# Kernel optimization log

Measured on AMD Instinct MI355X. Metric: run time of the kernel, lower is better.

## Reference

```python
import jax, jax.numpy as jnp
import numpy as np

EMBED = 1024
HEAD = 64
CTX = 2048


def setup_inputs() -> dict:
    key = jax.random.key(0)
    ks = jax.random.split(key, 7)
    scale = 1.0 / np.sqrt(EMBED)
    return {
        "x": jax.random.normal(ks[0], (8, CTX, EMBED), dtype=jnp.float32),
        "Wq": jax.random.normal(ks[1], (EMBED, HEAD), dtype=jnp.float32) * scale,
        "bq": jax.random.normal(ks[2], (HEAD,), dtype=jnp.float32) * 0.01,
        "Wk": jax.random.normal(ks[3], (EMBED, HEAD), dtype=jnp.float32) * scale,
        "bk": jax.random.normal(ks[4], (HEAD,), dtype=jnp.float32) * 0.01,
        "Wv": jax.random.normal(ks[5], (EMBED, HEAD), dtype=jnp.float32) * scale,
        "bv": jax.random.normal(ks[6], (HEAD,), dtype=jnp.float32) * 0.01,
    }


def reference(x, Wq, bq, Wk, bk, Wv, bv):
    # x: [B, T, E]
    q = x @ Wq + bq  # [B, T, H]
    k = x @ Wk + bk
    v = x @ Wv + bv
    scores = jnp.einsum("bqh,bkh->bqk", q, k) / jnp.sqrt(jnp.float32(HEAD))
    T = x.shape[1]
    causal = jnp.tril(jnp.ones((T, T), dtype=bool))
    scores = jnp.where(causal, scores, -jnp.inf)
    attn = jax.nn.softmax(scores, axis=-1)  # dropout=0.0 -> identity
    out = jnp.einsum("bqk,bkh->bqh", attn, v)
    return out
```

## Files before the change

### kernel.cpp

```cpp
#include <hip/hip_runtime.h>
#include <math.h>
#include <stdint.h>

#define BDIM 8
#define TDIM 2048
#define EDIM 1024
#define HDIM 64
#define NCHUNK 144

typedef short bf16x8 __attribute__((ext_vector_type(8)));
typedef float f32x4 __attribute__((ext_vector_type(4)));

__device__ __forceinline__ unsigned short f2bf(float f) {
    uint32_t u = __builtin_bit_cast(uint32_t, f);
    u += 0x7fffu + ((u >> 16) & 1u);
    return (unsigned short)(u >> 16);
}

__global__ __launch_bounds__(256) void prep_w(
    const float* __restrict__ Wq, const float* __restrict__ Wk,
    const float* __restrict__ Wv,
    unsigned short* __restrict__ WqT, unsigned short* __restrict__ WkT,
    unsigned short* __restrict__ WvT)
{
    int id = blockIdx.x * 256 + threadIdx.x;
    int e = id >> 6, h = id & 63;
    int oi = h * EDIM + e;
    WqT[oi] = f2bf(Wq[id]);
    WkT[oi] = f2bf(Wk[id]);
    WvT[oi] = f2bf(Wv[id]);
}

__global__ __launch_bounds__(256) void proj_kernel(
    const float* __restrict__ x,
    const unsigned short* __restrict__ WqT, const unsigned short* __restrict__ WkT,
    const unsigned short* __restrict__ WvT,
    const float* __restrict__ bq, const float* __restrict__ bk,
    const float* __restrict__ bv,
    unsigned short* __restrict__ Qb, unsigned short* __restrict__ Kb,
    unsigned short* __restrict__ VbT)
{
    __shared__ unsigned short Xs[2][64][72];
    __shared__ unsigned short Wqs[2][64][72];
    __shared__ unsigned short Wks[2][64][72];
    __shared__ unsigned short Wvs[2][64][72];

    const int t = threadIdx.x;
    const int lane = t & 63, w = t >> 6, quad = lane >> 4, ln = lane & 15;
    const int row0 = blockIdx.x * 64;
    const int sr = t >> 2;
    const int sc = (t & 3) << 4;

    f32x4 accq[4], acck[4], accv[4];
#pragma unroll
    for (int j = 0; j < 4; ++j) {
        accq[j] = (f32x4)(0.f); acck[j] = (f32x4)(0.f); accv[j] = (f32x4)(0.f);
    }

    const float*          xp0 = &x[(size_t)(row0 + sr) * EDIM + sc];
    const unsigned short* wp  = (const unsigned short*)0;
    const size_t wrow = (size_t)sr * EDIM + sc;

    {
        float4 x0 = *(const float4*)(xp0);
        float4 x1 = *(const float4*)(xp0 + 4);
        float4 x2 = *(const float4*)(xp0 + 8);
        float4 x3 = *(const float4*)(xp0 + 12);
        bf16x8 xb0, xb1;
        xb0[0]=(short)f2bf(x0.x); xb0[1]=(short)f2bf(x0.y); xb0[2]=(short)f2bf(x0.z); xb0[3]=(short)f2bf(x0.w);
        xb0[4]=(short)f2bf(x1.x); xb0[5]=(short)f2bf(x1.y); xb0[6]=(short)f2bf(x1.z); xb0[7]=(short)f2bf(x1.w);
        xb1[0]=(short)f2bf(x2.x); xb1[1]=(short)f2bf(x2.y); xb1[2]=(short)f2bf(x2.z); xb1[3]=(short)f2bf(x2.w);
        xb1[4]=(short)f2bf(x3.x); xb1[5]=(short)f2bf(x3.y); xb1[6]=(short)f2bf(x3.z); xb1[7]=(short)f2bf(x3.w);
        *(bf16x8*)&Xs[0][sr][sc]     = xb0;
        *(bf16x8*)&Xs[0][sr][sc + 8] = xb1;
        *(bf16x8*)&Wqs[0][sr][sc]     = *(const bf16x8*)&WqT[wrow];
        *(bf16x8*)&Wqs[0][sr][sc + 8] = *(const bf16x8*)&WqT[wrow + 8];
        *(bf16x8*)&Wks[0][sr][sc]     = *(const bf16x8*)&WkT[wrow];
        *(bf16x8*)&Wks[0][sr][sc + 8] = *(const bf16x8*)&WkT[wrow + 8];
        *(bf16x8*)&Wvs[0][sr][sc]     = *(const bf16x8*)&WvT[wrow];
        *(bf16x8*)&Wvs[0][sr][sc + 8] = *(const bf16x8*)&WvT[wrow + 8];
    }

    for (int kt = 0; kt < EDIM / 64; ++kt) {
        const int cur = kt & 1, nxt = cur ^ 1;

        float4 x0, x1, x2, x3;
        bf16x8 wq0, wq1, wk0, wk1, wv0, wv1;
        if (kt < 15) {
            const float* xp = xp0 + (kt + 1) * 64;
            x0 = *(const float4*)(xp);
            x1 = *(const float4*)(xp + 4);
            x2 = *(const float4*)(xp + 8);
            x3 = *(const float4*)(xp + 12);
            const size_t wo = wrow + (kt + 1) * 64;
            wq0 = *(const bf16x8*)&WqT[wo];
            wq1 = *(const bf16x8*)&WqT[wo + 8];
            wk0 = *(const bf16x8*)&WkT[wo];
            wk1 = *(const bf16x8*)&WkT[wo + 8];
            wv0 = *(const bf16x8*)&WvT[wo];
            wv1 = *(const bf16x8*)&WvT[wo + 8];
        }

        __syncthreads();

        bf16x8 xa0 = *(const bf16x8*)&Xs[cur][16 * w + ln][8 * quad];
        bf16x8 xa1 = *(const bf16x8*)&Xs[cur][16 * w + ln][32 + 8 * quad];
#pragma unroll
        for (int j = 0; j < 4; ++j) {
            bf16x8 w0, w1;
            w0 = *(const bf16x8*)&Wqs[cur][16 * j + ln][8 * quad];
            w1 = *(const bf16x8*)&Wqs[cur][16 * j + ln][32 + 8 * quad];
            accq[j] = __builtin_amdgcn_mfma_f32_16x16x32_bf16(xa0, w0, accq[j], 0, 0, 0);
            accq[j] = __builtin_amdgcn_mfma_f32_16x16x32_bf16(xa1, w1, accq[j], 0, 0, 0);
            w0 = *(const bf16x8*)&Wks[cur][16 * j + ln][8 * quad];
            w1 = *(const bf16x8*)&Wks[cur][16 * j + ln][32 + 8 * quad];
            acck[j] = __builtin_amdgcn_mfma_f32_16x16x32_bf16(xa0, w0, acck[j], 0, 0, 0);
            acck[j] = __builtin_amdgcn_mfma_f32_16x16x32_bf16(xa1, w1, acck[j], 0, 0, 0);
            w0 = *(const bf16x8*)&Wvs[cur][16 * j + ln][8 * quad];
            w1 = *(const bf16x8*)&Wvs[cur][16 * j + ln][32 + 8 * quad];
            accv[j] = __builtin_amdgcn_mfma_f32_16x16x32_bf16(xa0, w0, accv[j], 0, 0, 0);
            accv[j] = __builtin_amdgcn_mfma_f32_16x16x32_bf16(xa1, w1, accv[j], 0, 0, 0);
        }

        if (kt < 15) {
            bf16x8 xb0, xb1;
            xb0[0]=(short)f2bf(x0.x); xb0[1]=(short)f2bf(x0.y); xb0[2]=(short)f2bf(x0.z); xb0[3]=(short)f2bf(x0.w);
            xb0[4]=(short)f2bf(x1.x); xb0[5]=(short)f2bf(x1.y); xb0[6]=(short)f2bf(x1.z); xb0[7]=(short)f2bf(x1.w);
            xb1[0]=(short)f2bf(x2.x); xb1[1]=(short)f2bf(x2.y); xb1[2]=(short)f2bf(x2.z); xb1[3]=(short)f2bf(x2.w);
            xb1[4]=(short)f2bf(x3.x); xb1[5]=(short)f2bf(x3.y); xb1[6]=(short)f2bf(x3.z); xb1[7]=(short)f2bf(x3.w);
            *(bf16x8*)&Xs[nxt][sr][sc]     = xb0;
            *(bf16x8*)&Xs[nxt][sr][sc + 8] = xb1;
            *(bf16x8*)&Wqs[nxt][sr][sc]     = wq0;
            *(bf16x8*)&Wqs[nxt][sr][sc + 8] = wq1;
            *(bf16x8*)&Wks[nxt][sr][sc]     = wk0;
            *(bf16x8*)&Wks[nxt][sr][sc + 8] = wk1;
            *(bf16x8*)&Wvs[nxt][sr][sc]     = wv0;
            *(bf16x8*)&Wvs[nxt][sr][sc + 8] = wv1;
        }
    }

#pragma unroll
    for (int j = 0; j < 4; ++j) {
        int col = 16 * j + ln;
        float bqv = bq[col], bkv = bk[col], bvv = bv[col];
#pragma unroll
        for (int r = 0; r < 4; ++r) {
            size_t row = (size_t)(row0 + 16 * w + 4 * quad + r);
            Qb[row * HDIM + col] = f2bf(accq[j][r] + bqv);
            Kb[row * HDIM + col] = f2bf(acck[j][r] + bkv);
            int bb = (int)(row >> 11);
            int tr = (int)(row & 2047);
            VbT[((size_t)bb * HDIM + col) * TDIM + tr] = f2bf(accv[j][r] + bvv);
        }
    }
}

__global__ __launch_bounds__(256) void attn_partial(
    const unsigned short* __restrict__ Qb, const unsigned short* __restrict__ Kb,
    const unsigned short* __restrict__ VbT,
    float* __restrict__ PO, float* __restrict__ Pm, float* __restrict__ Pl)
{
    __shared__ unsigned short Ks[64][72];
    __shared__ unsigned short VsT[64][72];
    __shared__ unsigned short Ps[64][72];

    const int t = threadIdx.x;
    const int lane = t & 63, w = t >> 6, quad = lane >> 4, ln = lane & 15;
    const int f = blockIdx.x;
    const int b = blockIdx.y;

    int g = 0;
    while (f >= 2 * (g + 1) * (g + 2)) ++g;
    const int r_  = f - 2 * g * (g + 1);
    const int iq  = 4 * g + r_ / (g + 1);
    const int ch  = r_ % (g + 1);

    const int q0 = iq * 64;
    const size_t base = (size_t)b * TDIM * HDIM;
    const int sr = t >> 2;
    const int sc = (t & 3) << 4;

    const size_t qrow = base + (size_t)(q0 + 16 * w + ln) * HDIM;
    bf16x8 qa0 = *(const bf16x8*)&Qb[qrow + 8 * quad];
    bf16x8 qa1 = *(const bf16x8*)&Qb[qrow + 32 + 8 * quad];

    f32x4 od[4];
#pragma unroll
    for (int j = 0; j < 4; ++j) od[j] = (f32x4)(0.f);
    float mrow[4], lrow[4];
#pragma unroll
    for (int r = 0; r < 4; ++r) { mrow[r] = -INFINITY; lrow[r] = 0.f; }

    const float scale = 0.125f;
    int j1 = 4 * ch + 3; if (j1 > iq) j1 = iq;

    for (int jt = 4 * ch; jt <= j1; ++jt) {
        __syncthreads();
        {
            size_t ko = base + (size_t)(jt * 64 + sr) * HDIM + sc;
            *(bf16x8*)&Ks[sr][sc]     = *(const bf16x8*)&Kb[ko];
            *(bf16x8*)&Ks[sr][sc + 8] = *(const bf16x8*)&Kb[ko + 8];
            const unsigned short* vrow =
                &VbT[((size_t)b * HDIM + sr) * TDIM + jt * 64 + sc];
            *(bf16x8*)&VsT[sr][sc]     = *(const bf16x8*)vrow;
            *(bf16x8*)&VsT[sr][sc + 8] = *(const bf16x8*)(vrow + 8);
        }
        __syncthreads();

        f32x4 s[4];
#pragma unroll
        for (int j = 0; j < 4; ++j) {
            bf16x8 kb0 = *(const bf16x8*)&Ks[16 * j + ln][8 * quad];
            bf16x8 kb1 = *(const bf16x8*)&Ks[16 * j + ln][32 + 8 * quad];
            s[j] = (f32x4)(0.f);
            s[j] = __builtin_amdgcn_mfma_f32_16x16x32_bf16(qa0, kb0, s[j], 0, 0, 0);
            s[j] = __builtin_amdgcn_mfma_f32_16x16x32_bf16(qa1, kb1, s[j], 0, 0, 0);
        }

        if (jt == iq) {
#pragma unroll
            for (int j = 0; j < 4; ++j) {
                int kg = jt * 64 + 16 * j + ln;
#pragma unroll
                for (int r = 0; r < 4; ++r) {
                    int qg = q0 + 16 * w + 4 * quad + r;
                    s[j][r] = (kg <= qg) ? s[j][r] * scale : -INFINITY;
                }
            }
        } else {
#pragma unroll
            for (int j = 0; j < 4; ++j)
#pragma unroll
                for (int r = 0; r < 4; ++r) s[j][r] *= scale;
        }

        float mx[4];
#pragma unroll
        for (int r = 0; r < 4; ++r)
            mx[r] = fmaxf(fmaxf(s[0][r], s[1][r]), fmaxf(s[2][r], s[3][r]));
#pragma unroll
        for (int d = 1; d < 16; d <<= 1)
#pragma unroll
            for (int r = 0; r < 4; ++r)
                mx[r] = fmaxf(mx[r], __shfl_xor(mx[r], d));

        float al[4], rs[4];
#pragma unroll
        for (int r = 0; r < 4; ++r) {
            float mn = fmaxf(mrow[r], mx[r]);
            al[r] = __expf(mrow[r] - mn);
            mrow[r] = mn;
            float p0 = __expf(s[0][r] - mn);
            float p1 = __expf(s[1][r] - mn);
            float p2 = __expf(s[2][r] - mn);
            float p3 = __expf(s[3][r] - mn);
            s[0][r] = p0; s[1][r] = p1; s[2][r] = p2; s[3][r] = p3;
            rs[r] = (p0 + p1) + (p2 + p3);
        }
#pragma unroll
        for (int d = 1; d < 16; d <<= 1)
#pragma unroll
            for (int r = 0; r < 4; ++r)
                rs[r] += __shfl_xor(rs[r], d);
#pragma unroll
        for (int r = 0; r < 4; ++r) lrow[r] = lrow[r] * al[r] + rs[r];

#pragma unroll
        for (int j = 0; j < 4; ++j)
#pragma unroll
            for (int r = 0; r < 4; ++r) {
                od[j][r] *= al[r];
                Ps[16 * w + 4 * quad + r][16 * j + ln] = f2bf(s[j][r]);
            }

        bf16x8 pa0 = *(const bf16x8*)&Ps[16 * w + ln][8 * quad];
        bf16x8 pa1 = *(const bf16x8*)&Ps[16 * w + ln][32 + 8 * quad];
#pragma unroll
        for (int j = 0; j < 4; ++j) {
            bf16x8 vb0 = *(const bf16x8*)&VsT[16 * j + ln][8 * quad];
            bf16x8 vb1 = *(const bf16x8*)&VsT[16 * j + ln][32 + 8 * quad];
            od[j] = __builtin_amdgcn_mfma_f32_16x16x32_bf16(pa0, vb0, od[j], 0, 0, 0);
            od[j] = __builtin_amdgcn_mfma_f32_16x16x32_bf16(pa1, vb1, od[j], 0, 0, 0);
        }
    }

    const size_t p = (size_t)b * NCHUNK + f;
#pragma unroll
    for (int j = 0; j < 4; ++j)
#pragma unroll
        for (int r = 0; r < 4; ++r)
            PO[p * 4096 + (size_t)(16 * w + 4 * quad + r) * 64 + 16 * j + ln] = od[j][r];
    if (ln == 0) {
#pragma unroll
        for (int r = 0; r < 4; ++r) {
            Pm[p * 64 + 16 * w + 4 * quad + r] = mrow[r];
            Pl[p * 64 + 16 * w + 4 * quad + r] = lrow[r];
        }
    }
}

__global__ __launch_bounds__(256) void attn_combine(
    const float* __restrict__ PO, const float* __restrict__ Pm,
    const float* __restrict__ Pl, float* __restrict__ out)
{
    const int iq = blockIdx.x, b = blockIdx.y;
    const int g = iq >> 2;
    const int nch = g + 1;
    const int fbase = 2 * g * (g + 1) + (iq - 4 * g) * (g + 1);
    const int t = threadIdx.x;
    const int row = t >> 2;
    const int c0 = (t & 3) << 4;
    const size_t pbase = (size_t)b * NCHUNK + fbase;

    float M = -INFINITY;
    for (int c = 0; c < nch; ++c)
        M = fmaxf(M, Pm[(pbase + c) * 64 + row]);

    float4 a0 = {0,0,0,0}, a1 = {0,0,0,0}, a2 = {0,0,0,0}, a3 = {0,0,0,0};
    float L = 0.f;
    for (int c = 0; c < nch; ++c) {
        size_t p = pbase + c;
        float sc = __expf(Pm[p * 64 + row] - M);
        L += sc * Pl[p * 64 + row];
        const float* po = &PO[p * 4096 + (size_t)row * 64 + c0];
        float4 v0 = *(const float4*)(po);
        float4 v1 = *(const float4*)(po + 4);
        float4 v2 = *(const float4*)(po + 8);
        float4 v3 = *(const float4*)(po + 12);
        a0.x += sc*v0.x; a0.y += sc*v0.y; a0.z += sc*v0.z; a0.w += sc*v0.w;
        a1.x += sc*v1.x; a1.y += sc*v1.y; a1.z += sc*v1.z; a1.w += sc*v1.w;
        a2.x += sc*v2.x; a2.y += sc*v2.y; a2.z += sc*v2.z; a2.w += sc*v2.w;
        a3.x += sc*v3.x; a3.y += sc*v3.y; a3.z += sc*v3.z; a3.w += sc*v3.w;
    }
    float li = 1.f / L;
    a0.x*=li; a0.y*=li; a0.z*=li; a0.w*=li;
    a1.x*=li; a1.y*=li; a1.z*=li; a1.w*=li;
    a2.x*=li; a2.y*=li; a2.z*=li; a2.w*=li;
    a3.x*=li; a3.y*=li; a3.z*=li; a3.w*=li;
    float* op = &out[((size_t)b * TDIM + (size_t)iq * 64 + row) * HDIM + c0];
    *(float4*)(op)      = a0;
    *(float4*)(op + 4)  = a1;
    *(float4*)(op + 8)  = a2;
    *(float4*)(op + 12) = a3;
}

extern "C" void kernel_launch(void* const* d_in, const int* in_sizes, int n_in,
                              void* d_out, int out_size, void* d_ws, size_t ws_size,
                              hipStream_t stream) {
    const float* x  = (const float*)d_in[0];
    const float* Wq = (const float*)d_in[1];
    const float* bq = (const float*)d_in[2];
    const float* Wk = (const float*)d_in[3];
    const float* bk = (const float*)d_in[4];
    const float* Wv = (const float*)d_in[5];
    const float* bv = (const float*)d_in[6];
    float* out = (float*)d_out;

    const size_t n = (size_t)BDIM * TDIM * HDIM;
    unsigned short* Qb  = (unsigned short*)d_ws;
    unsigned short* Kb  = Qb + n;
    unsigned short* VbT = Kb + n;
    unsigned short* WqT = VbT + n;
    unsigned short* WkT = WqT + (size_t)EDIM * HDIM;
    unsigned short* WvT = WkT + (size_t)EDIM * HDIM;
    float* PO = (float*)(WvT + (size_t)EDIM * HDIM);
    float* Pm = PO + (size_t)BDIM * NCHUNK * 4096;
    float* Pl = Pm + (size_t)BDIM * NCHUNK * 64;

    prep_w<<<dim3(EDIM * HDIM / 256), 256, 0, stream>>>(Wq, Wk, Wv, WqT, WkT, WvT);
    proj_kernel<<<dim3(BDIM * TDIM / 64), 256, 0, stream>>>(
        x, WqT, WkT, WvT, bq, bk, bv, Qb, Kb, VbT);
    attn_partial<<<dim3(NCHUNK, BDIM), 256, 0, stream>>>(Qb, Kb, VbT, PO, Pm, Pl);
    attn_combine<<<dim3(TDIM / 64, BDIM), 256, 0, stream>>>(PO, Pm, Pl, out);
}
```

Before: 151.3 us.

## Split projection across Q/K/V blocks and store partial outputs in bf16

The projection kernel now launches three times as many blocks, each computing only one of Q, K or V for a 64-row tile. This cuts shared memory and registers per block and raises parallelism, but x is read and converted three times. Separately, the partial attention outputs are written as bf16 instead of fp32, halving the partial-output write and read traffic in the combine kernel at some cost in precision.

```diff
diff --git a/kernel.cpp b/kernel.cpp
--- a/kernel.cpp
+++ b/kernel.cpp
@@ -15,6 +15,10 @@
     uint32_t u = __builtin_bit_cast(uint32_t, f);
     u += 0x7fffu + ((u >> 16) & 1u);
     return (unsigned short)(u >> 16);
+}
+__device__ __forceinline__ float bf2f(unsigned short s) {
+    uint32_t u = ((uint32_t)s) << 16;
+    return __builtin_bit_cast(float, u);
 }
 
 __global__ __launch_bounds__(256) void prep_w(
@@ -41,24 +45,23 @@
     unsigned short* __restrict__ VbT)
 {
     __shared__ unsigned short Xs[2][64][72];
-    __shared__ unsigned short Wqs[2][64][72];
-    __shared__ unsigned short Wks[2][64][72];
-    __shared__ unsigned short Wvs[2][64][72];
+    __shared__ unsigned short Ws[2][64][72];
 
     const int t = threadIdx.x;
     const int lane = t & 63, w = t >> 6, quad = lane >> 4, ln = lane & 15;
-    const int row0 = blockIdx.x * 64;
+    const int which = blockIdx.x % 3;
+    const int row0  = (blockIdx.x / 3) * 64;
     const int sr = t >> 2;
     const int sc = (t & 3) << 4;
 
-    f32x4 accq[4], acck[4], accv[4];
-#pragma unroll
-    for (int j = 0; j < 4; ++j) {
-        accq[j] = (f32x4)(0.f); acck[j] = (f32x4)(0.f); accv[j] = (f32x4)(0.f);
-    }
-
-    const float*          xp0 = &x[(size_t)(row0 + sr) * EDIM + sc];
-    const unsigned short* wp  = (const unsigned short*)0;
+    const unsigned short* WT = (which == 0) ? WqT : (which == 1) ? WkT : WvT;
+    const float* bias        = (which == 0) ? bq  : (which == 1) ? bk  : bv;
+
+    f32x4 acc[4];
+#pragma unroll
+    for (int j = 0; j < 4; ++j) acc[j] = (f32x4)(0.f);
+
+    const float* xp0  = &x[(size_t)(row0 + sr) * EDIM + sc];
     const size_t wrow = (size_t)sr * EDIM + sc;
 
     {
@@ -73,19 +76,15 @@
         xb1[4]=(short)f2bf(x3.x); xb1[5]=(short)f2bf(x3.y); xb1[6]=(short)f2bf(x3.z); xb1[7]=(short)f2bf(x3.w);
         *(bf16x8*)&Xs[0][sr][sc]     = xb0;
         *(bf16x8*)&Xs[0][sr][sc + 8] = xb1;
-        *(bf16x8*)&Wqs[0][sr][sc]     = *(const bf16x8*)&WqT[wrow];
-        *(bf16x8*)&Wqs[0][sr][sc + 8] = *(const bf16x8*)&WqT[wrow + 8];
-        *(bf16x8*)&Wks[0][sr][sc]     = *(const bf16x8*)&WkT[wrow];
-        *(bf16x8*)&Wks[0][sr][sc + 8] = *(const bf16x8*)&WkT[wrow + 8];
-        *(bf16x8*)&Wvs[0][sr][sc]     = *(const bf16x8*)&WvT[wrow];
-        *(bf16x8*)&Wvs[0][sr][sc + 8] = *(const bf16x8*)&WvT[wrow + 8];
+        *(bf16x8*)&Ws[0][sr][sc]     = *(const bf16x8*)&WT[wrow];
+        *(bf16x8*)&Ws[0][sr][sc + 8] = *(const bf16x8*)&WT[wrow + 8];
     }
 
     for (int kt = 0; kt < EDIM / 64; ++kt) {
         const int cur = kt & 1, nxt = cur ^ 1;
 
         float4 x0, x1, x2, x3;
-        bf16x8 wq0, wq1, wk0, wk1, wv0, wv1;
+        bf16x8 wv0, wv1;
         if (kt < 15) {
             const float* xp = xp0 + (kt + 1) * 64;
             x0 = *(const float4*)(xp);
@@ -93,12 +92,8 @@
             x2 = *(const float4*)(xp + 8);
             x3 = *(const float4*)(xp + 12);
             const size_t wo = wrow + (kt + 1) * 64;
-            wq0 = *(const bf16x8*)&WqT[wo];
-            wq1 = *(const bf16x8*)&WqT[wo + 8];
-            wk0 = *(const bf16x8*)&WkT[wo];
-            wk1 = *(const bf16x8*)&WkT[wo + 8];
-            wv0 = *(const bf16x8*)&WvT[wo];
-            wv1 = *(const bf16x8*)&WvT[wo + 8];
+            wv0 = *(const bf16x8*)&WT[wo];
+            wv1 = *(const bf16x8*)&WT[wo + 8];
         }
 
         __syncthreads();
@@ -107,19 +102,10 @@
         bf16x8 xa1 = *(const bf16x8*)&Xs[cur][16 * w + ln][32 + 8 * quad];
 #pragma unroll
         for (int j = 0; j < 4; ++j) {
-            bf16x8 w0, w1;
-            w0 = *(const bf16x8*)&Wqs[cur][16 * j + ln][8 * quad];
-            w1 = *(const bf16x8*)&Wqs[cur][16 * j + ln][32 + 8 * quad];
-            accq[j] = __builtin_amdgcn_mfma_f32_16x16x32_bf16(xa0, w0, accq[j], 0, 0, 0);
-            accq[j] = __builtin_amdgcn_mfma_f32_16x16x32_bf16(xa1, w1, accq[j], 0, 0, 0);
-            w0 = *(const bf16x8*)&Wks[cur][16 * j + ln][8 * quad];
-            w1 = *(const bf16x8*)&Wks[cur][16 * j + ln][32 + 8 * quad];
-            acck[j] = __builtin_amdgcn_mfma_f32_16x16x32_bf16(xa0, w0, acck[j], 0, 0, 0);
-            acck[j] = __builtin_amdgcn_mfma_f32_16x16x32_bf16(xa1, w1, acck[j], 0, 0, 0);
-            w0 = *(const bf16x8*)&Wvs[cur][16 * j + ln][8 * quad];
-            w1 = *(const bf16x8*)&Wvs[cur][16 * j + ln][32 + 8 * quad];
-            accv[j] = __builtin_amdgcn_mfma_f32_16x16x32_bf16(xa0, w0, accv[j], 0, 0, 0);
-            accv[j] = __builtin_amdgcn_mfma_f32_16x16x32_bf16(xa1, w1, accv[j], 0, 0, 0);
+            bf16x8 w0 = *(const bf16x8*)&Ws[cur][16 * j + ln][8 * quad];
+            bf16x8 w1 = *(const bf16x8*)&Ws[cur][16 * j + ln][32 + 8 * quad];
+            acc[j] = __builtin_amdgcn_mfma_f32_16x16x32_bf16(xa0, w0, acc[j], 0, 0, 0);
+            acc[j] = __builtin_amdgcn_mfma_f32_16x16x32_bf16(xa1, w1, acc[j], 0, 0, 0);
         }
 
         if (kt < 15) {
@@ -130,27 +116,28 @@
             xb1[4]=(short)f2bf(x3.x); xb1[5]=(short)f2bf(x3.y); xb1[6]=(short)f2bf(x3.z); xb1[7]=(short)f2bf(x3.w);
             *(bf16x8*)&Xs[nxt][sr][sc]     = xb0;
             *(bf16x8*)&Xs[nxt][sr][sc + 8] = xb1;
-            *(bf16x8*)&Wqs[nxt][sr][sc]     = wq0;
-            *(bf16x8*)&Wqs[nxt][sr][sc + 8] = wq1;
-            *(bf16x8*)&Wks[nxt][sr][sc]     = wk0;
-            *(bf16x8*)&Wks[nxt][sr][sc + 8] = wk1;
-            *(bf16x8*)&Wvs[nxt][sr][sc]     = wv0;
-            *(bf16x8*)&Wvs[nxt][sr][sc + 8] = wv1;
+            *(bf16x8*)&Ws[nxt][sr][sc]     = wv0;
+            *(bf16x8*)&Ws[nxt][sr][sc + 8] = wv1;
         }
     }
 
 #pragma unroll
     for (int j = 0; j < 4; ++j) {
         int col = 16 * j + ln;
-        float bqv = bq[col], bkv = bk[col], bvv = bv[col];
+        float bv_ = bias[col];
 #pragma unroll
         for (int r = 0; r < 4; ++r) {
             size_t row = (size_t)(row0 + 16 * w + 4 * quad + r);
-            Qb[row * HDIM + col] = f2bf(accq[j][r] + bqv);
-            Kb[row * HDIM + col] = f2bf(acck[j][r] + bkv);
-            int bb = (int)(row >> 11);
-            int tr = (int)(row & 2047);
-            VbT[((size_t)bb * HDIM + col) * TDIM + tr] = f2bf(accv[j][r] + bvv);
+            unsigned short val = f2bf(acc[j][r] + bv_);
+            if (which == 0) {
+                Qb[row * HDIM + col] = val;
+            } else if (which == 1) {
+                Kb[row * HDIM + col] = val;
+            } else {
+                int bb = (int)(row >> 11);
+                int tr = (int)(row & 2047);
+                VbT[((size_t)bb * HDIM + col) * TDIM + tr] = val;
+            }
         }
     }
 }
@@ -158,7 +145,7 @@
 __global__ __launch_bounds__(256) void attn_partial(
     const unsigned short* __restrict__ Qb, const unsigned short* __restrict__ Kb,
     const unsigned short* __restrict__ VbT,
-    float* __restrict__ PO, float* __restrict__ Pm, float* __restrict__ Pl)
+    unsigned short* __restrict__ PO, float* __restrict__ Pm, float* __restrict__ Pl)
 {
     __shared__ unsigned short Ks[64][72];
     __shared__ unsigned short VsT[64][72];
@@ -289,7 +276,8 @@
     for (int j = 0; j < 4; ++j)
 #pragma unroll
         for (int r = 0; r < 4; ++r)
-            PO[p * 4096 + (size_t)(16 * w + 4 * quad + r) * 64 + 16 * j + ln] = od[j][r];
+            PO[p * 4096 + (size_t)(16 * w + 4 * quad + r) * 64 + 16 * j + ln] =
+                f2bf(od[j][r]);
     if (ln == 0) {
 #pragma unroll
         for (int r = 0; r < 4; ++r) {
@@ -300,7 +288,7 @@
 }
 
 __global__ __launch_bounds__(256) void attn_combine(
-    const float* __restrict__ PO, const float* __restrict__ Pm,
+    const unsigned short* __restrict__ PO, const float* __restrict__ Pm,
     const float* __restrict__ Pl, float* __restrict__ out)
 {
     const int iq = blockIdx.x, b = blockIdx.y;
@@ -316,32 +304,34 @@
     for (int c = 0; c < nch; ++c)
         M = fmaxf(M, Pm[(pbase + c) * 64 + row]);
 
-    float4 a0 = {0,0,0,0}, a1 = {0,0,0,0}, a2 = {0,0,0,0}, a3 = {0,0,0,0};
+    float a[16];
+#pragma unroll
+    for (int i = 0; i < 16; ++i) a[i] = 0.f;
     float L = 0.f;
     for (int c = 0; c < nch; ++c) {
         size_t p = pbase + c;
         float sc = __expf(Pm[p * 64 + row] - M);
         L += sc * Pl[p * 64 + row];
-        const float* po = &PO[p * 4096 + (size_t)row * 64 + c0];
-        float4 v0 = *(const float4*)(po);
-        float4 v1 = *(const float4*)(po + 4);
-        float4 v2 = *(const float4*)(po + 8);
-        float4 v3 = *(const float4*)(po + 12);
-        a0.x += sc*v0.x; a0.y += sc*v0.y; a0.z += sc*v0.z; a0.w += sc*v0.w;
-        a1.x += sc*v1.x; a1.y += sc*v1.y; a1.z += sc*v1.z; a1.w += sc*v1.w;
-        a2.x += sc*v2.x; a2.y += sc*v2.y; a2.z += sc*v2.z; a2.w += sc*v2.w;
-        a3.x += sc*v3.x; a3.y += sc*v3.y; a3.z += sc*v3.z; a3.w += sc*v3.w;
+        const unsigned short* po = &PO[p * 4096 + (size_t)row * 64 + c0];
+        bf16x8 v0 = *(const bf16x8*)(po);
+        bf16x8 v1 = *(const bf16x8*)(po + 8);
+#pragma unroll
+        for (int i = 0; i < 8; ++i) {
+            a[i]     += sc * bf2f((unsigned short)v0[i]);
+            a[8 + i] += sc * bf2f((unsigned short)v1[i]);
+        }
     }
     float li = 1.f / L;
-    a0.x*=li; a0.y*=li; a0.z*=li; a0.w*=li;
-    a1.x*=li; a1.y*=li; a1.z*=li; a1.w*=li;
-    a2.x*=li; a2.y*=li; a2.z*=li; a2.w*=li;
-    a3.x*=li; a3.y*=li; a3.z*=li; a3.w*=li;
+    float4 o0, o1, o2, o3;
+    o0.x=a[0]*li;  o0.y=a[1]*li;  o0.z=a[2]*li;  o0.w=a[3]*li;
+    o1.x=a[4]*li;  o1.y=a[5]*li;  o1.z=a[6]*li;  o1.w=a[7]*li;
+    o2.x=a[8]*li;  o2.y=a[9]*li;  o2.z=a[10]*li; o2.w=a[11]*li;
+    o3.x=a[12]*li; o3.y=a[13]*li; o3.z=a[14]*li; o3.w=a[15]*li;
     float* op = &out[((size_t)b * TDIM + (size_t)iq * 64 + row) * HDIM + c0];
-    *(float4*)(op)      = a0;
-    *(float4*)(op + 4)  = a1;
-    *(float4*)(op + 8)  = a2;
-    *(float4*)(op + 12) = a3;
+    *(float4*)(op)      = o0;
+    *(float4*)(op + 4)  = o1;
+    *(float4*)(op + 8)  = o2;
+    *(float4*)(op + 12) = o3;
 }
 
 extern "C" void kernel_launch(void* const* d_in, const int* in_sizes, int n_in,
@@ -363,12 +353,12 @@
     unsigned short* WqT = VbT + n;
     unsigned short* WkT = WqT + (size_t)EDIM * HDIM;
     unsigned short* WvT = WkT + (size_t)EDIM * HDIM;
-    float* PO = (float*)(WvT + (size_t)EDIM * HDIM);
-    float* Pm = PO + (size_t)BDIM * NCHUNK * 4096;
+    unsigned short* PO  = WvT + (size_t)EDIM * HDIM;
+    float* Pm = (float*)(PO + (size_t)BDIM * NCHUNK * 4096);
     float* Pl = Pm + (size_t)BDIM * NCHUNK * 64;
 
     prep_w<<<dim3(EDIM * HDIM / 256), 256, 0, stream>>>(Wq, Wk, Wv, WqT, WkT, WvT);
-    proj_kernel<<<dim3(BDIM * TDIM / 64), 256, 0, stream>>>(
+    proj_kernel<<<dim3(3 * BDIM * TDIM / 64), 256, 0, stream>>>(
         x, WqT, WkT, WvT, bq, bk, bv, Qb, Kb, VbT);
     attn_partial<<<dim3(NCHUNK, BDIM), 256, 0, stream>>>(Qb, Kb, VbT, PO, Pm, Pl);
     attn_combine<<<dim3(TDIM / 64, BDIM), 256, 0, stream>>>(PO, Pm, Pl, out);
```

After: 155.8 us. 1.03x slower.

## Double-buffer K/V tiles in attention and store partial outputs as bf16

Applied to the files above, without the earlier changes.

Attention partial kernel now prefetches the next K/V tile into registers and writes it to a second LDS buffer after the compute, removing one barrier per tile and overlapping global loads with MFMA work. Partial output accumulators are stored as bf16 instead of fp32, halving the write and read traffic between the partial and combine kernels. This costs some precision in the partial outputs and doubles K/V shared memory.

```diff
diff --git a/kernel.cpp b/kernel.cpp
--- a/kernel.cpp
+++ b/kernel.cpp
@@ -15,6 +15,10 @@
     uint32_t u = __builtin_bit_cast(uint32_t, f);
     u += 0x7fffu + ((u >> 16) & 1u);
     return (unsigned short)(u >> 16);
+}
+__device__ __forceinline__ float bf2f(unsigned short s) {
+    uint32_t u = ((uint32_t)s) << 16;
+    return __builtin_bit_cast(float, u);
 }
 
 __global__ __launch_bounds__(256) void prep_w(
@@ -57,8 +61,7 @@
         accq[j] = (f32x4)(0.f); acck[j] = (f32x4)(0.f); accv[j] = (f32x4)(0.f);
     }
 
-    const float*          xp0 = &x[(size_t)(row0 + sr) * EDIM + sc];
-    const unsigned short* wp  = (const unsigned short*)0;
+    const float* xp0  = &x[(size_t)(row0 + sr) * EDIM + sc];
     const size_t wrow = (size_t)sr * EDIM + sc;
 
     {
@@ -158,10 +161,10 @@
 __global__ __launch_bounds__(256) void attn_partial(
     const unsigned short* __restrict__ Qb, const unsigned short* __restrict__ Kb,
     const unsigned short* __restrict__ VbT,
-    float* __restrict__ PO, float* __restrict__ Pm, float* __restrict__ Pl)
+    unsigned short* __restrict__ PO, float* __restrict__ Pm, float* __restrict__ Pl)
 {
-    __shared__ unsigned short Ks[64][72];
-    __shared__ unsigned short VsT[64][72];
+    __shared__ unsigned short Ks[2][64][72];
+    __shared__ unsigned short VsT[2][64][72];
     __shared__ unsigned short Ps[64][72];
 
     const int t = threadIdx.x;
@@ -192,26 +195,40 @@
     for (int r = 0; r < 4; ++r) { mrow[r] = -INFINITY; lrow[r] = 0.f; }
 
     const float scale = 0.125f;
-    int j1 = 4 * ch + 3; if (j1 > iq) j1 = iq;
-
-    for (int jt = 4 * ch; jt <= j1; ++jt) {
+    const int jt0 = 4 * ch;
+    int j1 = jt0 + 3; if (j1 > iq) j1 = iq;
+
+    {
+        size_t ko = base + (size_t)(jt0 * 64 + sr) * HDIM + sc;
+        *(bf16x8*)&Ks[0][sr][sc]     = *(const bf16x8*)&Kb[ko];
+        *(bf16x8*)&Ks[0][sr][sc + 8] = *(const bf16x8*)&Kb[ko + 8];
+        const unsigned short* vrow =
+            &VbT[((size_t)b * HDIM + sr) * TDIM + jt0 * 64 + sc];
+        *(bf16x8*)&VsT[0][sr][sc]     = *(const bf16x8*)vrow;
+        *(bf16x8*)&VsT[0][sr][sc + 8] = *(const bf16x8*)(vrow + 8);
+    }
+
+    for (int jt = jt0; jt <= j1; ++jt) {
+        const int cur = (jt - jt0) & 1, nxt = cur ^ 1;
+
+        bf16x8 kn0, kn1, vn0, vn1;
+        if (jt < j1) {
+            size_t ko = base + (size_t)((jt + 1) * 64 + sr) * HDIM + sc;
+            kn0 = *(const bf16x8*)&Kb[ko];
+            kn1 = *(const bf16x8*)&Kb[ko + 8];
+            const unsigned short* vrow =
+                &VbT[((size_t)b * HDIM + sr) * TDIM + (jt + 1) * 64 + sc];
+            vn0 = *(const bf16x8*)vrow;
+            vn1 = *(const bf16x8*)(vrow + 8);
+        }
+
         __syncthreads();
-        {
-            size_t ko = base + (size_t)(jt * 64 + sr) * HDIM + sc;
-            *(bf16x8*)&Ks[sr][sc]     = *(const bf16x8*)&Kb[ko];
-            *(bf16x8*)&Ks[sr][sc + 8] = *(const bf16x8*)&Kb[ko + 8];
-            const unsigned short* vrow =
-                &VbT[((size_t)b * HDIM + sr) * TDIM + jt * 64 + sc];
-            *(bf16x8*)&VsT[sr][sc]     = *(const bf16x8*)vrow;
-            *(bf16x8*)&VsT[sr][sc + 8] = *(const bf16x8*)(vrow + 8);
-        }
-        __syncthreads();
 
         f32x4 s[4];
 #pragma unroll
         for (int j = 0; j < 4; ++j) {
-            bf16x8 kb0 = *(const bf16x8*)&Ks[16 * j + ln][8 * quad];
-            bf16x8 kb1 = *(const bf16x8*)&Ks[16 * j + ln][32 + 8 * quad];
+            bf16x8 kb0 = *(const bf16x8*)&Ks[cur][16 * j + ln][8 * quad];
+            bf16x8 kb1 = *(const bf16x8*)&Ks[cur][16 * j + ln][32 + 8 * quad];
             s[j] = (f32x4)(0.f);
             s[j] = __builtin_amdgcn_mfma_f32_16x16x32_bf16(qa0, kb0, s[j], 0, 0, 0);
             s[j] = __builtin_amdgcn_mfma_f32_16x16x32_bf16(qa1, kb1, s[j], 0, 0, 0);
@@ -277,11 +294,18 @@
         bf16x8 pa1 = *(const bf16x8*)&Ps[16 * w + ln][32 + 8 * quad];
 #pragma unroll
         for (int j = 0; j < 4; ++j) {
-            bf16x8 vb0 = *(const bf16x8*)&VsT[16 * j + ln][8 * quad];
-            bf16x8 vb1 = *(const bf16x8*)&VsT[16 * j + ln][32 + 8 * quad];
+            bf16x8 vb0 = *(const bf16x8*)&VsT[cur][16 * j + ln][8 * quad];
+            bf16x8 vb1 = *(const bf16x8*)&VsT[cur][16 * j + ln][32 + 8 * quad];
             od[j] = __builtin_amdgcn_mfma_f32_16x16x32_bf16(pa0, vb0, od[j], 0, 0, 0);
             od[j] = __builtin_amdgcn_mfma_f32_16x16x32_bf16(pa1, vb1, od[j], 0, 0, 0);
         }
+
+        if (jt < j1) {
+            *(bf16x8*)&Ks[nxt][sr][sc]     = kn0;
+            *(bf16x8*)&Ks[nxt][sr][sc + 8] = kn1;
+            *(bf16x8*)&VsT[nxt][sr][sc]     = vn0;
+            *(bf16x8*)&VsT[nxt][sr][sc + 8] = vn1;
+        }
     }
 
     const size_t p = (size_t)b * NCHUNK + f;
@@ -289,7 +313,8 @@
     for (int j = 0; j < 4; ++j)
 #pragma unroll
         for (int r = 0; r < 4; ++r)
-            PO[p * 4096 + (size_t)(16 * w + 4 * quad + r) * 64 + 16 * j + ln] = od[j][r];
+            PO[p * 4096 + (size_t)(16 * w + 4 * quad + r) * 64 + 16 * j + ln] =
+                f2bf(od[j][r]);
     if (ln == 0) {
 #pragma unroll
         for (int r = 0; r < 4; ++r) {
@@ -300,7 +325,7 @@
 }
 
 __global__ __launch_bounds__(256) void attn_combine(
-    const float* __restrict__ PO, const float* __restrict__ Pm,
+    const unsigned short* __restrict__ PO, const float* __restrict__ Pm,
     const float* __restrict__ Pl, float* __restrict__ out)
 {
     const int iq = blockIdx.x, b = blockIdx.y;
@@ -316,32 +341,34 @@
     for (int c = 0; c < nch; ++c)
         M = fmaxf(M, Pm[(pbase + c) * 64 + row]);
 
-    float4 a0 = {0,0,0,0}, a1 = {0,0,0,0}, a2 = {0,0,0,0}, a3 = {0,0,0,0};
+    float a[16];
+#pragma unroll
+    for (int i = 0; i < 16; ++i) a[i] = 0.f;
     float L = 0.f;
     for (int c = 0; c < nch; ++c) {
         size_t p = pbase + c;
         float sc = __expf(Pm[p * 64 + row] - M);
         L += sc * Pl[p * 64 + row];
-        const float* po = &PO[p * 4096 + (size_t)row * 64 + c0];
-        float4 v0 = *(const float4*)(po);
-        float4 v1 = *(const float4*)(po + 4);
-        float4 v2 = *(const float4*)(po + 8);
-        float4 v3 = *(const float4*)(po + 12);
-        a0.x += sc*v0.x; a0.y += sc*v0.y; a0.z += sc*v0.z; a0.w += sc*v0.w;
-        a1.x += sc*v1.x; a1.y += sc*v1.y; a1.z += sc*v1.z; a1.w += sc*v1.w;
-        a2.x += sc*v2.x; a2.y += sc*v2.y; a2.z += sc*v2.z; a2.w += sc*v2.w;
-        a3.x += sc*v3.x; a3.y += sc*v3.y; a3.z += sc*v3.z; a3.w += sc*v3.w;
+        const unsigned short* po = &PO[p * 4096 + (size_t)row * 64 + c0];
+        bf16x8 v0 = *(const bf16x8*)(po);
+        bf16x8 v1 = *(const bf16x8*)(po + 8);
+#pragma unroll
+        for (int i = 0; i < 8; ++i) {
+            a[i]     += sc * bf2f((unsigned short)v0[i]);
+            a[8 + i] += sc * bf2f((unsigned short)v1[i]);
+        }
     }
     float li = 1.f / L;
-    a0.x*=li; a0.y*=li; a0.z*=li; a0.w*=li;
-    a1.x*=li; a1.y*=li; a1.z*=li; a1.w*=li;
-    a2.x*=li; a2.y*=li; a2.z*=li; a2.w*=li;
-    a3.x*=li; a3.y*=li; a3.z*=li; a3.w*=li;
+    float4 o0, o1, o2, o3;
+    o0.x=a[0]*li;  o0.y=a[1]*li;  o0.z=a[2]*li;  o0.w=a[3]*li;
+    o1.x=a[4]*li;  o1.y=a[5]*li;  o1.z=a[6]*li;  o1.w=a[7]*li;
+    o2.x=a[8]*li;  o2.y=a[9]*li;  o2.z=a[10]*li; o2.w=a[11]*li;
+    o3.x=a[12]*li; o3.y=a[13]*li; o3.z=a[14]*li; o3.w=a[15]*li;
     float* op = &out[((size_t)b * TDIM + (size_t)iq * 64 + row) * HDIM + c0];
-    *(float4*)(op)      = a0;
-    *(float4*)(op + 4)  = a1;
-    *(float4*)(op + 8)  = a2;
-    *(float4*)(op + 12) = a3;
+    *(float4*)(op)      = o0;
+    *(float4*)(op + 4)  = o1;
+    *(float4*)(op + 8)  = o2;
+    *(float4*)(op + 12) = o3;
 }
 
 extern "C" void kernel_launch(void* const* d_in, const int* in_sizes, int n_in,
@@ -363,8 +390,8 @@
     unsigned short* WqT = VbT + n;
     unsigned short* WkT = WqT + (size_t)EDIM * HDIM;
     unsigned short* WvT = WkT + (size_t)EDIM * HDIM;
-    float* PO = (float*)(WvT + (size_t)EDIM * HDIM);
-    float* Pm = PO + (size_t)BDIM * NCHUNK * 4096;
+    unsigned short* PO  = WvT + (size_t)EDIM * HDIM;
+    float* Pm = (float*)(PO + (size_t)BDIM * NCHUNK * 4096);
     float* Pl = Pm + (size_t)BDIM * NCHUNK * 64;
 
     prep_w<<<dim3(EDIM * HDIM / 256), 256, 0, stream>>>(Wq, Wk, Wv, WqT, WkT, WvT);
```

Result: no change. 148.4 us (-1.9%).
